# Kernel optimization log

Hardware: AMD Instinct MI355X
Metric: run time of the kernel (lower is better)

## Reference

```python
import jax, jax.numpy as jnp
import numpy as np

B, L, N = 16, 512, 512
DM, DS, NL, DFF = 512, 16, 2, 2048
DI = 2 * DM          # expand=2
DCONV = 4
DTR = DM // 16       # dt_rank
H = 96
EPS = 1e-5


def _ln(x, w, b):
    m = jnp.mean(x, -1, keepdims=True)
    v = jnp.mean((x - m) ** 2, -1, keepdims=True)
    return (x - m) / jnp.sqrt(v + EPS) * w + b


def _mamba_dir(x, in_w, in_b, conv_w, conv_b, xp_w, dt_w, dt_b, A_log, Dp, out_w, out_b):
    # x: (B, S, DM)
    Bb, S, _ = x.shape
    xz = x @ in_w.T + in_b                       # (B,S,2*DI)
    u, z = jnp.split(xz, 2, -1)
    uc = jnp.swapaxes(u, 1, 2)                   # (B,DI,S)
    uc = jax.lax.conv_general_dilated(uc, conv_w[:, None, :], (1,), [(DCONV - 1, 0)],
                                      feature_group_count=DI,
                                      dimension_numbers=('NCH', 'OIH', 'NCH'))
    u = jax.nn.silu(jnp.swapaxes(uc + conv_b[None, :, None], 1, 2))  # (B,S,DI)
    x_dbl = u @ xp_w.T                           # (B,S,DTR+2*DS)
    dt, Bm, Cm = jnp.split(x_dbl, [DTR, DTR + DS], -1)
    delta = jax.nn.softplus(dt @ dt_w.T + dt_b)  # (B,S,DI)
    A = -jnp.exp(A_log)                          # (DI,DS)

    def step(h, inp):
        u_t, d_t, B_t, C_t = inp                 # (B,DI),(B,DI),(B,DS),(B,DS)
        h = jnp.exp(d_t[:, :, None] * A) * h + (d_t * u_t)[:, :, None] * B_t[:, None, :]
        return h, jnp.einsum('bds,bs->bd', h, C_t)

    h0 = jnp.zeros((Bb, DI, DS), x.dtype)
    _, ys = jax.lax.scan(step, h0, (jnp.swapaxes(u, 0, 1), jnp.swapaxes(delta, 0, 1),
                                    jnp.swapaxes(Bm, 0, 1), jnp.swapaxes(Cm, 0, 1)))
    y = jnp.swapaxes(ys, 0, 1) + u * Dp          # (B,S,DI)
    y = y * jax.nn.silu(z)
    return y @ out_w.T + out_b                   # (B,S,DM)


def _forward(x, tok_w, tok_b, in_w, in_b, conv_w, conv_b, xp_w, dt_w, dt_b, A_log, Dm,
             out_w, out_b, mnorm_w, mnorm_b, fnorm_w, fnorm_b, ffn_w1, ffn_b1, ffn_w2,
             ffn_b2, norm_w, norm_b, head_w, head_b):
    # RevIN: per-instance stats over time dim, no affine
    mu = jnp.mean(x, 1, keepdims=True)           # (B,1,N)
    sd = jnp.sqrt(jnp.var(x, 1, keepdims=True) + EPS)
    xn = (x - mu) / sd
    tokens = jnp.swapaxes(xn, 1, 2) @ tok_w.T + tok_b   # (B,N,DM) variate tokens
    for l in range(NL):
        yn = _ln(tokens, mnorm_w[l], mnorm_b[l])
        of = _mamba_dir(yn, in_w[l, 0], in_b[l, 0], conv_w[l, 0], conv_b[l, 0], xp_w[l, 0],
                        dt_w[l, 0], dt_b[l, 0], A_log[l, 0], Dm[l, 0], out_w[l, 0], out_b[l, 0])
        ob = _mamba_dir(yn[:, ::-1, :], in_w[l, 1], in_b[l, 1], conv_w[l, 1], conv_b[l, 1],
                        xp_w[l, 1], dt_w[l, 1], dt_b[l, 1], A_log[l, 1], Dm[l, 1],
                        out_w[l, 1], out_b[l, 1])[:, ::-1, :]
        tokens = tokens + of + ob                # bidirectional Mamba + residual
        res = tokens
        hdd = _ln(tokens, fnorm_w[l], fnorm_b[l])
        hdd = jax.nn.gelu(hdd @ ffn_w1[l].T + ffn_b1[l]) @ ffn_w2[l].T + ffn_b2[l]
        tokens = hdd + res
    tokens = _ln(tokens, norm_w, norm_b)
    pred = tokens @ head_w.T + head_b            # (B,N,H)
    pred = jnp.swapaxes(pred, 1, 2)              # (B,H,N)
    return pred * sd + mu                        # RevIN inverse


def setup_inputs() -> dict:
    key = jax.random.key(0)
    ks = jax.random.split(key, 12)
    def rn(k, shape, scale=0.02):
        return jax.random.normal(k, shape, jnp.float32) * scale
    return {
        'x': jax.random.normal(ks[0], (B, L, N), jnp.float32),
        'tok_w': rn(ks[1], (DM, L)), 'tok_b': jnp.zeros((DM,), jnp.float32),
        'in_w': rn(ks[2], (NL, 2, 2 * DI, DM)), 'in_b': jnp.zeros((NL, 2, 2 * DI), jnp.float32),
        'conv_w': rn(ks[3], (NL, 2, DI, DCONV), 0.2), 'conv_b': jnp.zeros((NL, 2, DI), jnp.float32),
        'xp_w': rn(ks[4], (NL, 2, DTR + 2 * DS, DI)),
        'dt_w': rn(ks[5], (NL, 2, DI, DTR)), 'dt_b': rn(ks[6], (NL, 2, DI), 0.1),
        'A_log': jnp.broadcast_to(jnp.log(jnp.arange(1., DS + 1.)), (NL, 2, DI, DS)).astype(jnp.float32),
        'Dm': jnp.ones((NL, 2, DI), jnp.float32),
        'out_w': rn(ks[7], (NL, 2, DM, DI)), 'out_b': jnp.zeros((NL, 2, DM), jnp.float32),
        'mnorm_w': jnp.ones((NL, DM), jnp.float32), 'mnorm_b': jnp.zeros((NL, DM), jnp.float32),
        'fnorm_w': jnp.ones((NL, DM), jnp.float32), 'fnorm_b': jnp.zeros((NL, DM), jnp.float32),
        'ffn_w1': rn(ks[8], (NL, DFF, DM)), 'ffn_b1': jnp.zeros((NL, DFF), jnp.float32),
        'ffn_w2': rn(ks[9], (NL, DM, DFF)), 'ffn_b2': jnp.zeros((NL, DM), jnp.float32),
        'norm_w': jnp.ones((DM,), jnp.float32), 'norm_b': jnp.zeros((DM,), jnp.float32),
        'head_w': rn(ks[10], (H, DM)), 'head_b': jnp.zeros((H,), jnp.float32),
    }


def reference(x, tok_w, tok_b, in_w, in_b, conv_w, conv_b, xp_w, dt_w, dt_b, A_log, Dm,
              out_w, out_b, mnorm_w, mnorm_b, fnorm_w, fnorm_b, ffn_w1, ffn_b1, ffn_w2,
              ffn_b2, norm_w, norm_b, head_w, head_b):
    return _forward(x, tok_w, tok_b, in_w, in_b, conv_w, conv_b, xp_w, dt_w, dt_b, A_log,
                    Dm, out_w, out_b, mnorm_w, mnorm_b, fnorm_w, fnorm_b, ffn_w1, ffn_b1,
                    ffn_w2, ffn_b2, norm_w, norm_b, head_w, head_b)
```

## Files before the change

### kernel.cpp

```cpp
#include <hip/hip_runtime.h>
#include <hip/hip_bf16.h>

#define Bb 16
#define Ll 512
#define NV 512
#define DM 512
#define DS 16
#define NLAY 2
#define DFF 2048
#define DI 1024
#define DCONV 4
#define DTR 32
#define Hh 96
#define Ss NV
#define MROWS (Bb*Ss)
#define EPSf 1e-5f
#define CH 32
#define NCH (Ss/CH)

typedef __hip_bfloat16 bf16;
typedef __attribute__((ext_vector_type(8))) short bf16x8;
typedef __attribute__((ext_vector_type(4))) float f32x4;

#define GLL16(g, l) __builtin_amdgcn_global_load_lds( \
    (const __attribute__((address_space(1))) unsigned int*)(g), \
    (__attribute__((address_space(3))) unsigned int*)(l), 16, 0, 0)

__device__ __forceinline__ float fast_exp(float x) { return __expf(x); }
__device__ __forceinline__ float fast_sig(float x) {
    return __builtin_amdgcn_rcpf(1.f + __expf(-x));
}
__device__ __forceinline__ float fast_softplus(float r) {
    float e = __expf(-fabsf(r));
    return fmaxf(r, 0.f) + __logf(1.f + e);
}
__device__ __forceinline__ float b2f(bf16 v) { return __bfloat162float(v); }

__global__ void f2bf(const float* __restrict__ in, bf16* __restrict__ out, int n) {
    int i = (blockIdx.x * 256 + threadIdx.x) * 4;
    if (i < n) {
        float4 v = *(const float4*)(in + i);
        out[i + 0] = __float2bfloat16(v.x);
        out[i + 1] = __float2bfloat16(v.y);
        out[i + 2] = __float2bfloat16(v.z);
        out[i + 3] = __float2bfloat16(v.w);
    }
}

__global__ void repack_outw(const float* __restrict__ outw, bf16* __restrict__ outwcat) {
    int idx = (blockIdx.x * 256 + threadIdx.x) * 4;
    int k2 = idx & 2047;
    int rest = idx >> 11;
    int l = rest >> 9, n = rest & 511;
    int dirk = k2 >> 10, k = k2 & 1023;
    const float* s = outw + (((size_t)(l * 2 + dirk) * DM + n) * DI + k);
    float4 v = *(const float4*)s;
    bf16* dpt = outwcat + (size_t)idx;
    dpt[0] = __float2bfloat16(v.x);
    dpt[1] = __float2bfloat16(v.y);
    dpt[2] = __float2bfloat16(v.z);
    dpt[3] = __float2bfloat16(v.w);
}

__global__ void sum_outb(const float* __restrict__ outb, float* __restrict__ outbsum) {
    int i = blockIdx.x * 256 + threadIdx.x;
    int l = i >> 9, n = i & 511;
    outbsum[i] = outb[(l * 2 + 0) * DM + n] + outb[(l * 2 + 1) * DM + n];
}

__global__ void revin_partial(const float* __restrict__ x, float* __restrict__ ps1,
                              float* __restrict__ ps2) {
    int b = blockIdx.x, c = blockIdx.y, n = threadIdx.x;
    const float* xp = x + (size_t)b * Ll * NV + (size_t)c * (Ll / 8) * NV + n;
    float s1 = 0.f, s2 = 0.f;
    #pragma unroll 4
    for (int l = 0; l < Ll / 8; l++) { float v = xp[(size_t)l * NV]; s1 += v; s2 += v * v; }
    ps1[((size_t)b * 8 + c) * NV + n] = s1;
    ps2[((size_t)b * 8 + c) * NV + n] = s2;
}

__global__ void revin_final(const float* __restrict__ ps1, const float* __restrict__ ps2,
                            float* __restrict__ mu, float* __restrict__ sd) {
    int b = blockIdx.x, n = threadIdx.x;
    float s1 = 0.f, s2 = 0.f;
    #pragma unroll
    for (int c = 0; c < 8; c++) {
        s1 += ps1[((size_t)b * 8 + c) * NV + n];
        s2 += ps2[((size_t)b * 8 + c) * NV + n];
    }
    float m = s1 / Ll;
    float var = s2 / Ll - m * m;
    mu[b * NV + n] = m;
    sd[b * NV + n] = sqrtf(var + EPSf);
}

__global__ void transpose_norm(const float* __restrict__ x, const float* __restrict__ mu,
                               const float* __restrict__ sd, bf16* __restrict__ xnT) {
    __shared__ float t[32][33];
    int b = blockIdx.z;
    int l0 = blockIdx.x * 32, n0 = blockIdx.y * 32;
    int tx = threadIdx.x, ty = threadIdx.y;
    #pragma unroll
    for (int q = 0; q < 4; q++)
        t[ty + q * 8][tx] = x[(size_t)b * Ll * NV + (size_t)(l0 + ty + q * 8) * NV + n0 + tx];
    __syncthreads();
    #pragma unroll
    for (int q = 0; q < 4; q++) {
        int n = n0 + ty + q * 8;
        float m = mu[b * NV + n], s = sd[b * NV + n];
        xnT[(size_t)b * NV * Ll + (size_t)n * Ll + l0 + tx] = __float2bfloat16((t[tx][ty + q * 8] - m) / s);
    }
}

__global__ void ln_rows(const float* __restrict__ in, const float* __restrict__ w,
                        const float* __restrict__ bvec, bf16* __restrict__ out) {
    int row = blockIdx.x;
    int tid = threadIdx.x;
    float v = in[(size_t)row * DM + tid];
    float s1 = v, s2 = v * v;
    #pragma unroll
    for (int o = 32; o > 0; o >>= 1) { s1 += __shfl_down(s1, o, 64); s2 += __shfl_down(s2, o, 64); }
    __shared__ float l1[8], l2[8];
    int wv = tid >> 6, ln = tid & 63;
    if (ln == 0) { l1[wv] = s1; l2[wv] = s2; }
    __syncthreads();
    if (tid == 0) {
        float a = 0.f, c = 0.f;
        #pragma unroll
        for (int i = 0; i < DM / 64; i++) { a += l1[i]; c += l2[i]; }
        l1[0] = a; l2[0] = c;
    }
    __syncthreads();
    float mean = l1[0] / DM;
    float var = l2[0] / DM - mean * mean;
    float inv = rsqrtf(var + EPSf);
    out[(size_t)row * DM + tid] = __float2bfloat16((v - mean) * inv * w[tid] + bvec[tid]);
}

template<int EPI, bool ACC, bool OUTBF>
__global__ __launch_bounds__(256) void gemm128(
    const bf16* __restrict__ A, int lda,
    const bf16* __restrict__ W,
    const float* __restrict__ bias,
    void* __restrict__ Cv, int ldc,
    int M, int Nn, int K) {
    __shared__ bf16 As[2][128 * 32];
    __shared__ bf16 Bs[2][128 * 32];
    int m0 = blockIdx.x * 128, n0 = blockIdx.y * 128;
    int tid = threadIdx.x;
    int w = tid >> 6, lane = tid & 63;
    int wm = (w >> 1) * 64, wn = (w & 1) * 64;
    f32x4 acc[4][4] = {};

    int srow = w * 32 + (lane >> 2);
    int sslot = (lane & 3) ^ ((lane >> 3) & 3);
    long arow0 = m0 + srow, arow1 = m0 + srow + 16;
    const char* agp0 = (const char*)(A + arow0 * (long)lda) + sslot * 16;
    const char* agp1 = (const char*)(A + arow1 * (long)lda) + sslot * 16;
    long wr0 = n0 + srow;      if (wr0 >= Nn) wr0 = Nn - 1;
    long wr1 = n0 + srow + 16; if (wr1 >= Nn) wr1 = Nn - 1;
    const char* wgp0 = (const char*)(W + wr0 * (long)K) + sslot * 16;
    const char* wgp1 = (const char*)(W + wr1 * (long)K) + sslot * 16;

    char* a0 = (char*)As[0]; char* a1 = (char*)As[1];
    char* b0 = (char*)Bs[0]; char* b1 = (char*)Bs[1];
    int dA0 = (w * 32) * 64, dA1 = (w * 32 + 16) * 64;

    int lrow = lane & 15;
    int salt = ((lane >> 4) ^ ((lane >> 1) & 3)) * 16;

    const int nk = K >> 5;
#define STG128(pa, pb, ko) do { \
        GLL16(agp0 + (size_t)(ko) * 64, pa + dA0); \
        GLL16(agp1 + (size_t)(ko) * 64, pa + dA1); \
        GLL16(wgp0 + (size_t)(ko) * 64, pb + dA0); \
        GLL16(wgp1 + (size_t)(ko) * 64, pb + dA1); } while (0)

    STG128(a0, b0, 0);
    __syncthreads();
    for (int t = 0; t < nk; ++t) {
        char* ac = (t & 1) ? a1 : a0;
        char* bc = (t & 1) ? b1 : b0;
        if (t + 1 < nk) {
            char* an = (t & 1) ? a0 : a1;
            char* bn = (t & 1) ? b0 : b1;
            STG128(an, bn, t + 1);
        }
        bf16x8 af[4], bfr[4];
        #pragma unroll
        for (int i = 0; i < 4; i++) {
            af[i]  = *(const bf16x8*)(ac + (wm + i * 16 + lrow) * 64 + salt);
            bfr[i] = *(const bf16x8*)(bc + (wn + i * 16 + lrow) * 64 + salt);
        }
        #pragma unroll
        for (int i = 0; i < 4; i++)
            #pragma unroll
            for (int j = 0; j < 4; j++)
                acc[i][j] = __builtin_amdgcn_mfma_f32_16x16x32_bf16(af[i], bfr[j], acc[i][j], 0, 0, 0);
        __syncthreads();
    }
#undef STG128

    #pragma unroll
    for (int i = 0; i < 4; i++) {
        #pragma unroll
        for (int j = 0; j < 4; j++) {
            int n = n0 + wn + j * 16 + (lane & 15);
            if (n >= Nn) continue;
            float bv = bias ? bias[n] : 0.f;
            #pragma unroll
            for (int r = 0; r < 4; r++) {
                long m = m0 + wm + i * 16 + (lane >> 4) * 4 + r;
                float v = acc[i][j][r] + bv;
                if (EPI == 1) {
                    float x3 = v * v * v;
                    v = 0.5f * v * (1.f + tanhf(0.7978845608028654f * (v + 0.044715f * x3)));
                }
                if (OUTBF) {
                    ((bf16*)Cv)[m * (long)ldc + n] = __float2bfloat16(v);
                } else if (ACC) {
                    ((float*)Cv)[m * (long)ldc + n] += v;
                } else {
                    ((float*)Cv)[m * (long)ldc + n] = v;
                }
            }
        }
    }
}

template<int EPI, bool ACC, bool OUTBF, int MT>
__global__ __launch_bounds__(256) void gemm64(
    const bf16* __restrict__ A, int lda,
    const bf16* __restrict__ W,
    const float* __restrict__ bias,
    void* __restrict__ Cv, int ldc,
    int M, int Nn, int K) {
    constexpr int WR = MT / 4;
    constexpr int IF = MT / 64;
    constexpr int AG = WR / 8;
    __shared__ bf16 As[2][MT * 64];
    __shared__ bf16 Bs[2][64 * 64];
    int m0 = blockIdx.x * MT, n0 = blockIdx.y * 64;
    int tid = threadIdx.x;
    int w = tid >> 6, lane = tid & 63;
    int wm = w * WR;
    f32x4 acc[IF][4] = {};

    int srow = lane >> 3;
    int sslot = (lane & 7) ^ srow;
    const char* agp[AG];
    #pragma unroll
    for (int g = 0; g < AG; g++) {
        long ar = m0 + w * WR + g * 8 + srow;
        agp[g] = (const char*)(A + ar * (long)lda) + sslot * 16;
    }
    const char* wgp[2];
    #pragma unroll
    for (int g = 0; g < 2; g++) {
        long br = n0 + w * 16 + g * 8 + srow;
        if (br >= Nn) br = Nn - 1;
        wgp[g] = (const char*)(W + br * (long)K) + sslot * 16;
    }
    char* a0 = (char*)As[0]; char* a1 = (char*)As[1];
    char* b0 = (char*)Bs[0]; char* b1 = (char*)Bs[1];

    int lrow = lane & 15;
    int rk = lane & 7, hi = lane >> 4;
    int salt0 = (hi ^ rk) * 16;
    int salt1 = ((4 + hi) ^ rk) * 16;

    const int nk = K >> 6;
#define STG64(pa, pb, ko) do { \
        _Pragma("unroll") \
        for (int g = 0; g < AG; g++) \
            GLL16(agp[g] + (size_t)(ko) * 128, pa + (w * WR + g * 8) * 128); \
        _Pragma("unroll") \
        for (int g = 0; g < 2; g++) \
            GLL16(wgp[g] + (size_t)(ko) * 128, pb + (w * 16 + g * 8) * 128); } while (0)

    STG64(a0, b0, 0);
    __syncthreads();
    for (int t = 0; t < nk; ++t) {
        char* ac = (t & 1) ? a1 : a0;
        char* bc = (t & 1) ? b1 : b0;
        if (t + 1 < nk) {
            char* an = (t & 1) ? a0 : a1;
            char* bn = (t & 1) ? b0 : b1;
            STG64(an, bn, t + 1);
        }
        bf16x8 af[2][IF], bfr[2][4];
        #pragma unroll
        for (int i = 0; i < IF; i++) {
            af[0][i] = *(const bf16x8*)(ac + (wm + i * 16 + lrow) * 128 + salt0);
            af[1][i] = *(const bf16x8*)(ac + (wm + i * 16 + lrow) * 128 + salt1);
        }
        #pragma unroll
        for (int j = 0; j < 4; j++) {
            bfr[0][j] = *(const bf16x8*)(bc + (j * 16 + lrow) * 128 + salt0);
            bfr[1][j] = *(const bf16x8*)(bc + (j * 16 + lrow) * 128 + salt1);
        }
        #pragma unroll
        for (int kk = 0; kk < 2; kk++)
            #pragma unroll
            for (int i = 0; i < IF; i++)
                #pragma unroll
                for (int j = 0; j < 4; j++)
                    acc[i][j] = __builtin_amdgcn_mfma_f32_16x16x32_bf16(af[kk][i], bfr[kk][j], acc[i][j], 0, 0, 0);
        __syncthreads();
    }
#undef STG64

    #pragma unroll
    for (int i = 0; i < IF; i++) {
        #pragma unroll
        for (int j = 0; j < 4; j++) {
            int n = n0 + j * 16 + (lane & 15);
            if (n >= Nn) continue;
            float bv = bias ? bias[n] : 0.f;
            #pragma unroll
            for (int r = 0; r < 4; r++) {
                long m = m0 + wm + i * 16 + (lane >> 4) * 4 + r;
                float v = acc[i][j][r] + bv;
                if (EPI == 1) {
                    float x3 = v * v * v;
                    v = 0.5f * v * (1.f + tanhf(0.7978845608028654f * (v + 0.044715f * x3)));
                }
                if (OUTBF) {
                    ((bf16*)Cv)[m * (long)ldc + n] = __float2bfloat16(v);
                } else if (ACC) {
                    ((float*)Cv)[m * (long)ldc + n] += v;
                } else {
                    ((float*)Cv)[m * (long)ldc + n] = v;
                }
            }
        }
    }
}

template<int EPI, bool ACC>
__global__ __launch_bounds__(256) void gemm_awt(
    const float* __restrict__ A, int lda,
    const float* __restrict__ W,
    const float* __restrict__ bias,
    float* __restrict__ C, int ldc,
    int M, int Nn, int K) {
    __shared__ float Asm[16][68];
    __shared__ float Wsm[16][68];
    int m0 = blockIdx.x * 64;
    int n0 = blockIdx.y * 64;
    int tid = threadIdx.x;
    int tm = (tid / 16) * 4, tn = (tid % 16) * 4;
    float acc[4][4] = {};
    int lr = tid / 4;
    int lk = (tid % 4) * 4;
    const float* aptr = A + (size_t)(m0 + lr) * lda + lk;
    int wrow = n0 + lr;
    bool wok = wrow < Nn;
    const float* wptr = W + (size_t)wrow * K + lk;
    for (int k0 = 0; k0 < K; k0 += 16) {
        float4 av = *(const float4*)(aptr + k0);
        float4 wv = wok ? *(const float4*)(wptr + k0) : make_float4(0.f, 0.f, 0.f, 0.f);
        Asm[lk + 0][lr] = av.x; Asm[lk + 1][lr] = av.y; Asm[lk + 2][lr] = av.z; Asm[lk + 3][lr] = av.w;
        Wsm[lk + 0][lr] = wv.x; Wsm[lk + 1][lr] = wv.y; Wsm[lk + 2][lr] = wv.z; Wsm[lk + 3][lr] = wv.w;
        __syncthreads();
        #pragma unroll
        for (int kk = 0; kk < 16; kk++) {
            float4 a = *(const float4*)&Asm[kk][tm];
            float4 wv2 = *(const float4*)&Wsm[kk][tn];
            float ar[4] = {a.x, a.y, a.z, a.w};
            float wr[4] = {wv2.x, wv2.y, wv2.z, wv2.w};
            #pragma unroll
            for (int i = 0; i < 4; i++)
                #pragma unroll
                for (int j = 0; j < 4; j++)
                    acc[i][j] = fmaf(ar[i], wr[j], acc[i][j]);
        }
        __syncthreads();
    }
    #pragma unroll
    for (int i = 0; i < 4; i++) {
        int m = m0 + tm + i;
        #pragma unroll
        for (int j = 0; j < 4; j++) {
            int n = n0 + tn + j;
            if (n < Nn) {
                float r = acc[i][j];
                if (bias) r += bias[n];
                if (EPI == 2) r = fast_softplus(r);
                if (ACC) C[(size_t)m * ldc + n] += r;
                else     C[(size_t)m * ldc + n] = r;
            }
        }
    }
}

__global__ void conv_both(const bf16* __restrict__ xz, const float* __restrict__ cw_l,
                          const float* __restrict__ cb_l, bf16* __restrict__ ub) {
    int c2 = blockIdx.x * 256 + threadIdx.x;
    int dir = c2 >> 10, c = c2 & 1023;
    int s0 = blockIdx.y * 16;
    int b = blockIdx.z;
    const bf16* src = xz + (size_t)b * Ss * 4096 + (size_t)dir * 2048 + c;
    const float* cw = cw_l + (dir * DI + c) * 4;
    float w0 = cw[0], w1 = cw[1], w2 = cw[2], w3 = cw[3];
    float bias = cb_l[dir * DI + c];
    bf16* dst = ub + (size_t)b * Ss * 2048 + (size_t)dir * 1024 + c;
    if (dir == 0) {
        float r0 = (s0 - 3 >= 0) ? b2f(src[(size_t)(s0 - 3) * 4096]) : 0.f;
        float r1 = (s0 - 2 >= 0) ? b2f(src[(size_t)(s0 - 2) * 4096]) : 0.f;
        float r2 = (s0 - 1 >= 0) ? b2f(src[(size_t)(s0 - 1) * 4096]) : 0.f;
        for (int i = 0; i < 16; i++) {
            int s = s0 + i;
            float r3 = b2f(src[(size_t)s * 4096]);
            float a = fmaf(r0, w0, fmaf(r1, w1, fmaf(r2, w2, fmaf(r3, w3, bias))));
            dst[(size_t)s * 2048] = __float2bfloat16(a * fast_sig(a));
            r0 = r1; r1 = r2; r2 = r3;
        }
    } else {
        float f0 = b2f(src[(size_t)s0 * 4096]);
        float f1 = (s0 + 1 < Ss) ? b2f(src[(size_t)(s0 + 1) * 4096]) : 0.f;
        float f2 = (s0 + 2 < Ss) ? b2f(src[(size_t)(s0 + 2) * 4096]) : 0.f;
        float f3 = (s0 + 3 < Ss) ? b2f(src[(size_t)(s0 + 3) * 4096]) : 0.f;
        for (int i = 0; i < 16; i++) {
            int s = s0 + i;
            float a = fmaf(f0, w3, fmaf(f1, w2, fmaf(f2, w1, fmaf(f3, w0, bias))));
            dst[(size_t)s * 2048] = __float2bfloat16(a * fast_sig(a));
            f0 = f1; f1 = f2; f2 = f3;
            f3 = (s + 4 < Ss) ? b2f(src[(size_t)(s + 4) * 4096]) : 0.f;
        }
    }
}

template<bool REV>
__global__ __launch_bounds__(256) void scan_pass1(
    const float* __restrict__ delta,
    const bf16* __restrict__ ub,
    const float* __restrict__ xdbl,
    const float* __restrict__ A_log,
    float* __restrict__ PB, float* __restrict__ HB) {
    int d = blockIdx.x * 256 + threadIdx.x;
    int c = blockIdx.y;
    int b = blockIdx.z;
    float Aj[DS], h[DS];
    #pragma unroll
    for (int j = 0; j < DS; j++) { Aj[j] = -fast_exp(A_log[(size_t)d * DS + j]); h[j] = 0.f; }
    float dlsum = 0.f;
    for (int i = 0; i < CH; i++) {
        int t = c * CH + i;
        int p = REV ? (Ss - 1 - t) : t;
        size_t row = (size_t)b * Ss + p;
        float dl = delta[row * DI + d];
        float ut = b2f(ub[row * 2048 + d]);
        float du = dl * ut;
        dlsum += dl;
        const float4* q4 = (const float4*)(xdbl + row * 64 + DTR);
        float4 B0 = q4[0], B1 = q4[1], B2 = q4[2], B3 = q4[3];
        float Bv[DS] = {B0.x, B0.y, B0.z, B0.w, B1.x, B1.y, B1.z, B1.w,
                        B2.x, B2.y, B2.z, B2.w, B3.x, B3.y, B3.z, B3.w};
        #pragma unroll
        for (int j = 0; j < DS; j++) {
            float a = fast_exp(dl * Aj[j]);
            h[j] = fmaf(a, h[j], du * Bv[j]);
        }
    }
    size_t base = ((size_t)(b * NCH + c)) * DS * DI + d;
    #pragma unroll
    for (int j = 0; j < DS; j++) {
        PB[base + (size_t)j * DI] = fast_exp(dlsum * Aj[j]);
        HB[base + (size_t)j * DI] = h[j];
    }
}

__global__ __launch_bounds__(256) void scan_pass2(
    const float* PB, const float* HB, float* HIN) {
    int idx = blockIdx.x * 256 + threadIdx.x;
    int b = idx >> 14;
    int rem = idx & 16383;
    float h = 0.f;
    #pragma unroll
    for (int c = 0; c < NCH; c++) {
        size_t o = ((size_t)(b * NCH + c)) * (DS * DI) + rem;
        float p = PB[o];
        float hl = HB[o];
        HIN[o] = h;
        h = fmaf(p, h, hl);
    }
}

template<bool REV>
__global__ __launch_bounds__(256) void scan_pass3(
    const float* __restrict__ delta,
    const bf16* __restrict__ ub,
    const float* __restrict__ xdbl,
    const bf16* __restrict__ zb,
    const float* __restrict__ A_log, const float* __restrict__ Dp,
    const float* __restrict__ HIN,
    bf16* __restrict__ yb) {
    int d = blockIdx.x * 256 + threadIdx.x;
    int c = blockIdx.y;
    int b = blockIdx.z;
    float Aj[DS], h[DS];
    size_t hbase = ((size_t)(b * NCH + c)) * DS * DI + d;
    #pragma unroll
    for (int j = 0; j < DS; j++) {
        Aj[j] = -fast_exp(A_log[(size_t)d * DS + j]);
        h[j] = HIN[hbase + (size_t)j * DI];
    }
    float Dd = Dp[d];
    for (int i = 0; i < CH; i++) {
        int t = c * CH + i;
        int p = REV ? (Ss - 1 - t) : t;
        size_t row = (size_t)b * Ss + p;
        float dl = delta[row * DI + d];
        float ut = b2f(ub[row * 2048 + d]);
        float zz = b2f(zb[row * 4096 + d]);
        float du = dl * ut;
        const float4* q4 = (const float4*)(xdbl + row * 64 + DTR);
        float4 B0 = q4[0], B1 = q4[1], B2 = q4[2], B3 = q4[3];
        float4 C0 = q4[4], C1 = q4[5], C2 = q4[6], C3 = q4[7];
        float Bv[DS] = {B0.x, B0.y, B0.z, B0.w, B1.x, B1.y, B1.z, B1.w,
                        B2.x, B2.y, B2.z, B2.w, B3.x, B3.y, B3.z, B3.w};
        float Cv[DS] = {C0.x, C0.y, C0.z, C0.w, C1.x, C1.y, C1.z, C1.w,
                        C2.x, C2.y, C2.z, C2.w, C3.x, C3.y, C3.z, C3.w};
        float acc = 0.f;
        #pragma unroll
        for (int j = 0; j < DS; j++) {
            float a = fast_exp(dl * Aj[j]);
            h[j] = fmaf(a, h[j], du * Bv[j]);
            acc = fmaf(h[j], Cv[j], acc);
        }
        float sg = fast_sig(zz);
        yb[row * 2048 + d] = __float2bfloat16((acc + ut * Dd) * (zz * sg));
    }
}

__global__ void finalize_out(const float* __restrict__ pred, const float* __restrict__ mu,
                             const float* __restrict__ sd, float* __restrict__ out) {
    int n = threadIdx.x;
    int h = blockIdx.x;
    int b = blockIdx.y;
    out[((size_t)b * Hh + h) * NV + n] =
        pred[((size_t)b * NV + n) * Hh + h] * sd[b * NV + n] + mu[b * NV + n];
}

extern "C" void kernel_launch(void* const* d_in, const int* in_sizes, int n_in,
                              void* d_out, int out_size, void* d_ws, size_t ws_size,
                              hipStream_t stream) {
    const float* x     = (const float*)d_in[0];
    const float* tokw  = (const float*)d_in[1];
    const float* tokb  = (const float*)d_in[2];
    const float* in_w  = (const float*)d_in[3];
    const float* in_b  = (const float*)d_in[4];
    const float* convw = (const float*)d_in[5];
    const float* convb = (const float*)d_in[6];
    const float* xpw   = (const float*)d_in[7];
    const float* dtw   = (const float*)d_in[8];
    const float* dtb   = (const float*)d_in[9];
    const float* Alog  = (const float*)d_in[10];
    const float* Dm    = (const float*)d_in[11];
    const float* outw  = (const float*)d_in[12];
    const float* outb  = (const float*)d_in[13];
    const float* mnw   = (const float*)d_in[14];
    const float* mnb   = (const float*)d_in[15];
    const float* fnw   = (const float*)d_in[16];
    const float* fnb   = (const float*)d_in[17];
    const float* fw1   = (const float*)d_in[18];
    const float* fb1   = (const float*)d_in[19];
    const float* fw2   = (const float*)d_in[20];
    const float* fb2   = (const float*)d_in[21];
    const float* nw    = (const float*)d_in[22];
    const float* nb    = (const float*)d_in[23];
    const float* hw    = (const float*)d_in[24];
    const float* hb    = (const float*)d_in[25];

    float* ws = (float*)d_ws;
    float* MU   = ws;
    float* SD   = MU + Bb * NV;
    float* R1   = SD + Bb * NV;
    float* T    = R1 + 2 * 1024 * 1024;
    float* YNR  = T + 4 * 1024 * 1024;
    float* XZR  = YNR + 2 * 1024 * 1024;
    float* UBR  = XZR + 16 * 1024 * 1024;
    float* DEL  = UBR + 8 * 1024 * 1024;
    float* PB   = DEL + 8 * 1024 * 1024;
    float* HB   = PB + 4 * 1024 * 1024;
    float* YBR  = HB + 4 * 1024 * 1024;
    float* WBF  = YBR + 8 * 1024 * 1024;

    bf16* XNTb = (bf16*)R1;
    float* XD  = R1;
    bf16* YNb  = (bf16*)YNR;
    bf16* XZb  = (bf16*)XZR;
    bf16* Ub   = (bf16*)UBR;
    bf16* Yb   = (bf16*)YBR;
    float* HIN = PB;
    float* PRED = DEL;

    bf16* wb = (bf16*)WBF;
    bf16* tokwb  = wb;  wb += (size_t)DM * Ll;
    bf16* inwb   = wb;  wb += (size_t)NLAY * 2 * 2 * DI * DM;
    bf16* xpwb   = wb;  wb += (size_t)NLAY * 2 * 64 * DI;
    bf16* outwc  = wb;  wb += (size_t)NLAY * DM * 2 * DI;
    bf16* fw1b   = wb;  wb += (size_t)NLAY * DFF * DM;
    bf16* fw2b   = wb;  wb += (size_t)NLAY * DM * DFF;
    bf16* hwb    = wb;  wb += (size_t)Hh * DM;
    float* outbsum = (float*)wb;
    float* PS1   = outbsum + NLAY * DM;
    float* PS2   = PS1 + Bb * 8 * NV;

    f2bf<<<(DM * Ll) / 1024, 256, 0, stream>>>(tokw, tokwb, DM * Ll);
    f2bf<<<(NLAY * 2 * 2 * DI * DM) / 1024, 256, 0, stream>>>(in_w, inwb, NLAY * 2 * 2 * DI * DM);
    f2bf<<<(NLAY * 2 * 64 * DI) / 1024, 256, 0, stream>>>(xpw, xpwb, NLAY * 2 * 64 * DI);
    repack_outw<<<(NLAY * DM * 2 * DI) / 1024, 256, 0, stream>>>(outw, outwc);
    sum_outb<<<(NLAY * DM) / 256, 256, 0, stream>>>(outb, outbsum);
    f2bf<<<(NLAY * DFF * DM) / 1024, 256, 0, stream>>>(fw1, fw1b, NLAY * DFF * DM);
    f2bf<<<(NLAY * DM * DFF) / 1024, 256, 0, stream>>>(fw2, fw2b, NLAY * DM * DFF);
    f2bf<<<(Hh * DM) / 1024, 256, 0, stream>>>(hw, hwb, Hh * DM);

    revin_partial<<<dim3(Bb, 8), NV, 0, stream>>>(x, PS1, PS2);
    revin_final<<<Bb, NV, 0, stream>>>(PS1, PS2, MU, SD);
    transpose_norm<<<dim3(Ll / 32, NV / 32, Bb), dim3(32, 8), 0, stream>>>(x, MU, SD, XNTb);
    gemm64<0, false, false, 128><<<dim3(MROWS / 128, DM / 64), 256, 0, stream>>>(
        XNTb, Ll, tokwb, tokb, T, DM, MROWS, DM, Ll);

    for (int l = 0; l < NLAY; l++) {
        ln_rows<<<MROWS, DM, 0, stream>>>(T, mnw + l * DM, mnb + l * DM, YNb);
        gemm128<0, false, true><<<dim3(MROWS / 128, 4096 / 128), 256, 0, stream>>>(
            YNb, DM, inwb + (size_t)l * 2 * 2 * DI * DM, in_b + (size_t)l * 2 * 2 * DI,
            XZb, 4096, MROWS, 4096, DM);
        conv_both<<<dim3(8, Ss / 16, Bb), 256, 0, stream>>>(
            XZb, convw + (size_t)l * 2 * DI * DCONV, convb + (size_t)l * 2 * DI, Ub);
        for (int dir = 0; dir < 2; dir++) {
            int pd = l * 2 + dir;
            gemm64<0, false, false, 64><<<dim3(MROWS / 64, 1), 256, 0, stream>>>(
                Ub + dir * 1024, 2 * DI, xpwb + (size_t)pd * 64 * DI, nullptr,
                XD, 64, MROWS, 64, DI);
            gemm_awt<2, false><<<dim3(MROWS / 64, DI / 64), 256, 0, stream>>>(
                XD, 64, dtw + (size_t)pd * DI * DTR, dtb + (size_t)pd * DI, DEL, DI,
                MROWS, DI, DTR);
            if (dir == 0) {
                scan_pass1<false><<<dim3(DI / 256, NCH, Bb), 256, 0, stream>>>(
                    DEL, Ub, XD, Alog + (size_t)pd * DI * DS, PB, HB);
                scan_pass2<<<(Bb * DS * DI) / 256, 256, 0, stream>>>(PB, HB, HIN);
                scan_pass3<false><<<dim3(DI / 256, NCH, Bb), 256, 0, stream>>>(
                    DEL, Ub, XD, XZb + 1024, Alog + (size_t)pd * DI * DS,
                    Dm + (size_t)pd * DI, HIN, Yb);
            } else {
                scan_pass1<true><<<dim3(DI / 256, NCH, Bb), 256, 0, stream>>>(
                    DEL, Ub + 1024, XD, Alog + (size_t)pd * DI * DS, PB, HB);
                scan_pass2<<<(Bb * DS * DI) / 256, 256, 0, stream>>>(PB, HB, HIN);
                scan_pass3<true><<<dim3(DI / 256, NCH, Bb), 256, 0, stream>>>(
                    DEL, Ub + 1024, XD, XZb + 2048 + 1024, Alog + (size_t)pd * DI * DS,
                    Dm + (size_t)pd * DI, HIN, Yb + 1024);
            }
        }
        gemm64<0, true, false, 128><<<dim3(MROWS / 128, DM / 64), 256, 0, stream>>>(
            Yb, 2 * DI, outwc + (size_t)l * DM * 2 * DI, outbsum + l * DM,
            T, DM, MROWS, DM, 2 * DI);
        ln_rows<<<MROWS, DM, 0, stream>>>(T, fnw + l * DM, fnb + l * DM, YNb);
        gemm128<1, false, true><<<dim3(MROWS / 128, DFF / 128), 256, 0, stream>>>(
            YNb, DM, fw1b + (size_t)l * DFF * DM, fb1 + l * DFF, XZb, DFF, MROWS, DFF, DM);
        gemm64<0, true, false, 128><<<dim3(MROWS / 128, DM / 64), 256, 0, stream>>>(
            XZb, DFF, fw2b + (size_t)l * DM * DFF, fb2 + l * DM, T, DM, MROWS, DM, DFF);
    }
    ln_rows<<<MROWS, DM, 0, stream>>>(T, nw, nb, YNb);
    gemm64<0, false, false, 64><<<dim3(MROWS / 64, 2), 256, 0, stream>>>(
        YNb, DM, hwb, hb, PRED, Hh, MROWS, Hh, DM);
    finalize_out<<<dim3(Hh, Bb), NV, 0, stream>>>(PRED, MU, SD, (float*)d_out);
}
```

Before: 942.2 us.

## Merge both scan directions into single launches with block-diagonal bf16 projection GEMMs

Builds block-diagonal bf16 weights so the x_proj and dt_proj GEMMs for both directions run as one wide MFMA GEMM each. Softplus moves into the gemm64 epilogue and delta is stored as bf16. The three scan passes now cover both directions in one launch, and the scan chunk size doubles to 64. This cuts the launch count, removes the fp32 SIMT dt GEMM and halves delta traffic, but the zero-padded K wastes GEMM work and bf16 delta lowers precision.

Result: no change. 931.7 us (-1.1%).

```diff
diff --git a/kernel.cpp b/kernel.cpp
--- a/kernel.cpp
+++ b/kernel.cpp
@@ -15,7 +15,7 @@
 #define Ss NV
 #define MROWS (Bb*Ss)
 #define EPSf 1e-5f
-#define CH 32
+#define CH 64
 #define NCH (Ss/CH)
 
 typedef __hip_bfloat16 bf16;
@@ -66,6 +66,27 @@
     int i = blockIdx.x * 256 + threadIdx.x;
     int l = i >> 9, n = i & 511;
     outbsum[i] = outb[(l * 2 + 0) * DM + n] + outb[(l * 2 + 1) * DM + n];
+}
+
+__global__ void build_xpw2(const float* __restrict__ xpw, bf16* __restrict__ out) {
+    int idx = blockIdx.x * 256 + threadIdx.x;
+    int l = idx >> 18;
+    int rest = idx & 262143;
+    int n = rest >> 11, k = rest & 2047;
+    int dir = n >> 6, nn = n & 63;
+    float v = ((k >> 10) == dir) ? xpw[((size_t)(l * 2 + dir) * 64 + nn) * DI + (k & 1023)] : 0.f;
+    out[idx] = __float2bfloat16(v);
+}
+
+__global__ void build_dtw2(const float* __restrict__ dtw, bf16* __restrict__ out) {
+    int idx = blockIdx.x * 256 + threadIdx.x;
+    int l = idx >> 18;
+    int rest = idx & 262143;
+    int n = rest >> 7, k = rest & 127;
+    int dir = n >> 10, nn = n & 1023;
+    int r = k - dir * 64;
+    float v = (r >= 0 && r < DTR) ? dtw[((size_t)(l * 2 + dir) * DI + nn) * DTR + r] : 0.f;
+    out[idx] = __float2bfloat16(v);
 }
 
 __global__ void revin_partial(const float* __restrict__ x, float* __restrict__ ps1,
@@ -324,6 +345,8 @@
                 if (EPI == 1) {
                     float x3 = v * v * v;
                     v = 0.5f * v * (1.f + tanhf(0.7978845608028654f * (v + 0.044715f * x3)));
+                } else if (EPI == 2) {
+                    v = fast_softplus(v);
                 }
                 if (OUTBF) {
                     ((bf16*)Cv)[m * (long)ldc + n] = __float2bfloat16(v);
@@ -332,63 +355,6 @@
                 } else {
                     ((float*)Cv)[m * (long)ldc + n] = v;
                 }
-            }
-        }
-    }
-}
-
-template<int EPI, bool ACC>
-__global__ __launch_bounds__(256) void gemm_awt(
-    const float* __restrict__ A, int lda,
-    const float* __restrict__ W,
-    const float* __restrict__ bias,
-    float* __restrict__ C, int ldc,
-    int M, int Nn, int K) {
-    __shared__ float Asm[16][68];
-    __shared__ float Wsm[16][68];
-    int m0 = blockIdx.x * 64;
-    int n0 = blockIdx.y * 64;
-    int tid = threadIdx.x;
-    int tm = (tid / 16) * 4, tn = (tid % 16) * 4;
-    float acc[4][4] = {};
-    int lr = tid / 4;
-    int lk = (tid % 4) * 4;
-    const float* aptr = A + (size_t)(m0 + lr) * lda + lk;
-    int wrow = n0 + lr;
-    bool wok = wrow < Nn;
-    const float* wptr = W + (size_t)wrow * K + lk;
-    for (int k0 = 0; k0 < K; k0 += 16) {
-        float4 av = *(const float4*)(aptr + k0);
-        float4 wv = wok ? *(const float4*)(wptr + k0) : make_float4(0.f, 0.f, 0.f, 0.f);
-        Asm[lk + 0][lr] = av.x; Asm[lk + 1][lr] = av.y; Asm[lk + 2][lr] = av.z; Asm[lk + 3][lr] = av.w;
-        Wsm[lk + 0][lr] = wv.x; Wsm[lk + 1][lr] = wv.y; Wsm[lk + 2][lr] = wv.z; Wsm[lk + 3][lr] = wv.w;
-        __syncthreads();
-        #pragma unroll
-        for (int kk = 0; kk < 16; kk++) {
-            float4 a = *(const float4*)&Asm[kk][tm];
-            float4 wv2 = *(const float4*)&Wsm[kk][tn];
-            float ar[4] = {a.x, a.y, a.z, a.w};
-            float wr[4] = {wv2.x, wv2.y, wv2.z, wv2.w};
-            #pragma unroll
-            for (int i = 0; i < 4; i++)
-                #pragma unroll
-                for (int j = 0; j < 4; j++)
-                    acc[i][j] = fmaf(ar[i], wr[j], acc[i][j]);
-        }
-        __syncthreads();
-    }
-    #pragma unroll
-    for (int i = 0; i < 4; i++) {
-        int m = m0 + tm + i;
-        #pragma unroll
-        for (int j = 0; j < 4; j++) {
-            int n = n0 + tn + j;
-            if (n < Nn) {
-                float r = acc[i][j];
-                if (bias) r += bias[n];
-                if (EPI == 2) r = fast_softplus(r);
-                if (ACC) C[(size_t)m * ldc + n] += r;
-                else     C[(size_t)m * ldc + n] = r;
             }
         }
     }
@@ -431,29 +397,30 @@
     }
 }
 
-template<bool REV>
 __global__ __launch_bounds__(256) void scan_pass1(
-    const float* __restrict__ delta,
+    const bf16* __restrict__ delb,
     const bf16* __restrict__ ub,
-    const float* __restrict__ xdbl,
-    const float* __restrict__ A_log,
+    const float* __restrict__ xd,
+    const float* __restrict__ Alog_l,
     float* __restrict__ PB, float* __restrict__ HB) {
-    int d = blockIdx.x * 256 + threadIdx.x;
+    int d2 = blockIdx.x * 256 + threadIdx.x;
+    int dir = d2 >> 10, d = d2 & 1023;
     int c = blockIdx.y;
     int b = blockIdx.z;
     float Aj[DS], h[DS];
-    #pragma unroll
-    for (int j = 0; j < DS; j++) { Aj[j] = -fast_exp(A_log[(size_t)d * DS + j]); h[j] = 0.f; }
+    const float* al = Alog_l + ((size_t)dir * DI + d) * DS;
+    #pragma unroll
+    for (int j = 0; j < DS; j++) { Aj[j] = -fast_exp(al[j]); h[j] = 0.f; }
     float dlsum = 0.f;
     for (int i = 0; i < CH; i++) {
         int t = c * CH + i;
-        int p = REV ? (Ss - 1 - t) : t;
+        int p = dir ? (Ss - 1 - t) : t;
         size_t row = (size_t)b * Ss + p;
-        float dl = delta[row * DI + d];
-        float ut = b2f(ub[row * 2048 + d]);
+        float dl = b2f(delb[row * 2048 + d2]);
+        float ut = b2f(ub[row * 2048 + d2]);
         float du = dl * ut;
         dlsum += dl;
-        const float4* q4 = (const float4*)(xdbl + row * 64 + DTR);
+        const float4* q4 = (const float4*)(xd + row * 128 + dir * 64 + DTR);
         float4 B0 = q4[0], B1 = q4[1], B2 = q4[2], B3 = q4[3];
         float Bv[DS] = {B0.x, B0.y, B0.z, B0.w, B1.x, B1.y, B1.z, B1.w,
                         B2.x, B2.y, B2.z, B2.w, B3.x, B3.y, B3.z, B3.w};
@@ -463,23 +430,23 @@
             h[j] = fmaf(a, h[j], du * Bv[j]);
         }
     }
-    size_t base = ((size_t)(b * NCH + c)) * DS * DI + d;
+    size_t base = ((size_t)(b * NCH + c) * DS) * 2048 + d2;
     #pragma unroll
     for (int j = 0; j < DS; j++) {
-        PB[base + (size_t)j * DI] = fast_exp(dlsum * Aj[j]);
-        HB[base + (size_t)j * DI] = h[j];
+        PB[base + (size_t)j * 2048] = fast_exp(dlsum * Aj[j]);
+        HB[base + (size_t)j * 2048] = h[j];
     }
 }
 
 __global__ __launch_bounds__(256) void scan_pass2(
     const float* PB, const float* HB, float* HIN) {
     int idx = blockIdx.x * 256 + threadIdx.x;
-    int b = idx >> 14;
-    int rem = idx & 16383;
+    int b = idx >> 15;
+    int rem = idx & 32767;
     float h = 0.f;
     #pragma unroll
     for (int c = 0; c < NCH; c++) {
-        size_t o = ((size_t)(b * NCH + c)) * (DS * DI) + rem;
+        size_t o = ((size_t)(b * NCH + c)) * 32768 + rem;
         float p = PB[o];
         float hl = HB[o];
         HIN[o] = h;
@@ -487,35 +454,36 @@
     }
 }
 
-template<bool REV>
 __global__ __launch_bounds__(256) void scan_pass3(
-    const float* __restrict__ delta,
+    const bf16* __restrict__ delb,
     const bf16* __restrict__ ub,
-    const float* __restrict__ xdbl,
-    const bf16* __restrict__ zb,
-    const float* __restrict__ A_log, const float* __restrict__ Dp,
+    const float* __restrict__ xd,
+    const bf16* __restrict__ xzb,
+    const float* __restrict__ Alog_l, const float* __restrict__ Dm_l,
     const float* __restrict__ HIN,
     bf16* __restrict__ yb) {
-    int d = blockIdx.x * 256 + threadIdx.x;
+    int d2 = blockIdx.x * 256 + threadIdx.x;
+    int dir = d2 >> 10, d = d2 & 1023;
     int c = blockIdx.y;
     int b = blockIdx.z;
     float Aj[DS], h[DS];
-    size_t hbase = ((size_t)(b * NCH + c)) * DS * DI + d;
+    const float* al = Alog_l + ((size_t)dir * DI + d) * DS;
+    size_t hbase = ((size_t)(b * NCH + c) * DS) * 2048 + d2;
     #pragma unroll
     for (int j = 0; j < DS; j++) {
-        Aj[j] = -fast_exp(A_log[(size_t)d * DS + j]);
-        h[j] = HIN[hbase + (size_t)j * DI];
-    }
-    float Dd = Dp[d];
+        Aj[j] = -fast_exp(al[j]);
+        h[j] = HIN[hbase + (size_t)j * 2048];
+    }
+    float Dd = Dm_l[dir * DI + d];
     for (int i = 0; i < CH; i++) {
         int t = c * CH + i;
-        int p = REV ? (Ss - 1 - t) : t;
+        int p = dir ? (Ss - 1 - t) : t;
         size_t row = (size_t)b * Ss + p;
-        float dl = delta[row * DI + d];
-        float ut = b2f(ub[row * 2048 + d]);
-        float zz = b2f(zb[row * 4096 + d]);
+        float dl = b2f(delb[row * 2048 + d2]);
+        float ut = b2f(ub[row * 2048 + d2]);
+        float zz = b2f(xzb[row * 4096 + dir * 2048 + 1024 + d]);
         float du = dl * ut;
-        const float4* q4 = (const float4*)(xdbl + row * 64 + DTR);
+        const float4* q4 = (const float4*)(xd + row * 128 + dir * 64 + DTR);
         float4 B0 = q4[0], B1 = q4[1], B2 = q4[2], B3 = q4[3];
         float4 C0 = q4[4], C1 = q4[5], C2 = q4[6], C3 = q4[7];
         float Bv[DS] = {B0.x, B0.y, B0.z, B0.w, B1.x, B1.y, B1.z, B1.w,
@@ -530,7 +498,7 @@
             acc = fmaf(h[j], Cv[j], acc);
         }
         float sg = fast_sig(zz);
-        yb[row * 2048 + d] = __float2bfloat16((acc + ut * Dd) * (zz * sg));
+        yb[row * 2048 + d2] = __float2bfloat16((acc + ut * Dd) * (zz * sg));
     }
 }
 
@@ -581,25 +549,28 @@
     float* YNR  = T + 4 * 1024 * 1024;
     float* XZR  = YNR + 2 * 1024 * 1024;
     float* UBR  = XZR + 16 * 1024 * 1024;
-    float* DEL  = UBR + 8 * 1024 * 1024;
-    float* PB   = DEL + 8 * 1024 * 1024;
+    float* DELR = UBR + 8 * 1024 * 1024;
+    float* PB   = DELR + 8 * 1024 * 1024;
     float* HB   = PB + 4 * 1024 * 1024;
     float* YBR  = HB + 4 * 1024 * 1024;
     float* WBF  = YBR + 8 * 1024 * 1024;
 
     bf16* XNTb = (bf16*)R1;
     float* XD  = R1;
+    bf16* XDb  = (bf16*)(R1 + 1024 * 1024);
     bf16* YNb  = (bf16*)YNR;
     bf16* XZb  = (bf16*)XZR;
     bf16* Ub   = (bf16*)UBR;
+    bf16* DELb = (bf16*)DELR;
     bf16* Yb   = (bf16*)YBR;
     float* HIN = PB;
-    float* PRED = DEL;
+    float* PRED = DELR;
 
     bf16* wb = (bf16*)WBF;
     bf16* tokwb  = wb;  wb += (size_t)DM * Ll;
     bf16* inwb   = wb;  wb += (size_t)NLAY * 2 * 2 * DI * DM;
-    bf16* xpwb   = wb;  wb += (size_t)NLAY * 2 * 64 * DI;
+    bf16* xpw2b  = wb;  wb += (size_t)NLAY * 128 * 2048;
+    bf16* dtw2b  = wb;  wb += (size_t)NLAY * 2048 * 128;
     bf16* outwc  = wb;  wb += (size_t)NLAY * DM * 2 * DI;
     bf16* fw1b   = wb;  wb += (size_t)NLAY * DFF * DM;
     bf16* fw2b   = wb;  wb += (size_t)NLAY * DM * DFF;
@@ -610,7 +581,8 @@
 
     f2bf<<<(DM * Ll) / 1024, 256, 0, stream>>>(tokw, tokwb, DM * Ll);
     f2bf<<<(NLAY * 2 * 2 * DI * DM) / 1024, 256, 0, stream>>>(in_w, inwb, NLAY * 2 * 2 * DI * DM);
-    f2bf<<<(NLAY * 2 * 64 * DI) / 1024, 256, 0, stream>>>(xpw, xpwb, NLAY * 2 * 64 * DI);
+    build_xpw2<<<(NLAY * 128 * 2048) / 256, 256, 0, stream>>>(xpw, xpw2b);
+    build_dtw2<<<(NLAY * 2048 * 128) / 256, 256, 0, stream>>>(dtw, dtw2b);
     repack_outw<<<(NLAY * DM * 2 * DI) / 1024, 256, 0, stream>>>(outw, outwc);
     sum_outb<<<(NLAY * DM) / 256, 256, 0, stream>>>(outb, outbsum);
     f2bf<<<(NLAY * DFF * DM) / 1024, 256, 0, stream>>>(fw1, fw1b, NLAY * DFF * DM);
@@ -630,30 +602,18 @@
             XZb, 4096, MROWS, 4096, DM);
         conv_both<<<dim3(8, Ss / 16, Bb), 256, 0, stream>>>(
             XZb, convw + (size_t)l * 2 * DI * DCONV, convb + (size_t)l * 2 * DI, Ub);
-        for (int dir = 0; dir < 2; dir++) {
-            int pd = l * 2 + dir;
-            gemm64<0, false, false, 64><<<dim3(MROWS / 64, 1), 256, 0, stream>>>(
-                Ub + dir * 1024, 2 * DI, xpwb + (size_t)pd * 64 * DI, nullptr,
-                XD, 64, MROWS, 64, DI);
-            gemm_awt<2, false><<<dim3(MROWS / 64, DI / 64), 256, 0, stream>>>(
-                XD, 64, dtw + (size_t)pd * DI * DTR, dtb + (size_t)pd * DI, DEL, DI,
-                MROWS, DI, DTR);
-            if (dir == 0) {
-                scan_pass1<false><<<dim3(DI / 256, NCH, Bb), 256, 0, stream>>>(
-                    DEL, Ub, XD, Alog + (size_t)pd * DI * DS, PB, HB);
-                scan_pass2<<<(Bb * DS * DI) / 256, 256, 0, stream>>>(PB, HB, HIN);
-                scan_pass3<false><<<dim3(DI / 256, NCH, Bb), 256, 0, stream>>>(
-                    DEL, Ub, XD, XZb + 1024, Alog + (size_t)pd * DI * DS,
-                    Dm + (size_t)pd * DI, HIN, Yb);
-            } else {
-                scan_pass1<true><<<dim3(DI / 256, NCH, Bb), 256, 0, stream>>>(
-                    DEL, Ub + 1024, XD, Alog + (size_t)pd * DI * DS, PB, HB);
-                scan_pass2<<<(Bb * DS * DI) / 256, 256, 0, stream>>>(PB, HB, HIN);
-                scan_pass3<true><<<dim3(DI / 256, NCH, Bb), 256, 0, stream>>>(
-                    DEL, Ub + 1024, XD, XZb + 2048 + 1024, Alog + (size_t)pd * DI * DS,
-                    Dm + (size_t)pd * DI, HIN, Yb + 1024);
-            }
-        }
+        gemm64<0, false, false, 64><<<dim3(MROWS / 64, 2), 256, 0, stream>>>(
+            Ub, 2048, xpw2b + (size_t)l * 128 * 2048, nullptr, XD, 128, MROWS, 128, 2048);
+        f2bf<<<(MROWS * 128) / 1024, 256, 0, stream>>>(XD, XDb, MROWS * 128);
+        gemm64<2, false, true, 128><<<dim3(MROWS / 128, 2048 / 64), 256, 0, stream>>>(
+            XDb, 128, dtw2b + (size_t)l * 2048 * 128, dtb + (size_t)l * 2 * DI,
+            DELb, 2048, MROWS, 2048, 128);
+        scan_pass1<<<dim3(2048 / 256, NCH, Bb), 256, 0, stream>>>(
+            DELb, Ub, XD, Alog + (size_t)l * 2 * DI * DS, PB, HB);
+        scan_pass2<<<(Bb * DS * 2048) / 256, 256, 0, stream>>>(PB, HB, HIN);
+        scan_pass3<<<dim3(2048 / 256, NCH, Bb), 256, 0, stream>>>(
+            DELb, Ub, XD, XZb, Alog + (size_t)l * 2 * DI * DS, Dm + (size_t)l * 2 * DI,
+            HIN, Yb);
         gemm64<0, true, false, 128><<<dim3(MROWS / 128, DM / 64), 256, 0, stream>>>(
             Yb, 2 * DI, outwc + (size_t)l * DM * 2 * DI, outbsum + l * DM,
             T, DM, MROWS, DM, 2 * DI);
```
